# Optimization experiments

Hardware: AMD Instinct MI355X
Metric: run time of the kernel (lower is better)

The kernel has to match this reference:

```python
import jax, jax.numpy as jnp
import numpy as np

B, S, D_MODEL, N_HEADS, D_HEAD = 2, 2048, 2048, 16, 128


def _rope_tables(seq_len, d_head, base=10000.0):
    # standard llama RoPE cos/sin tables, broadcastable to (B, H, S, d_head)
    inv_freq = 1.0 / (base ** (np.arange(0, d_head, 2, dtype=np.float32) / d_head))
    t = np.arange(seq_len, dtype=np.float32)
    freqs = np.outer(t, inv_freq)                      # (S, d_head/2)
    emb = np.concatenate([freqs, freqs], axis=-1)       # (S, d_head)
    cos = jnp.asarray(np.cos(emb))[None, None]          # (1,1,S,d_head)
    sin = jnp.asarray(np.sin(emb))[None, None]
    return cos, sin


def setup_inputs() -> dict:
    key = jax.random.key(0)
    ks = jax.random.split(key, 5)
    scale = 0.02
    x = jax.random.normal(ks[0], (B, S, D_MODEL), dtype=jnp.float32)
    Wq = jax.random.normal(ks[1], (D_MODEL, D_MODEL), dtype=jnp.float32) * scale
    Wk = jax.random.normal(ks[2], (D_MODEL, D_MODEL), dtype=jnp.float32) * scale
    Wv = jax.random.normal(ks[3], (D_MODEL, D_MODEL), dtype=jnp.float32) * scale
    Wo = jax.random.normal(ks[4], (D_MODEL, D_MODEL), dtype=jnp.float32) * scale
    cos, sin = _rope_tables(S, D_HEAD)
    return {"x": x, "cos": cos, "sin": sin, "Wq": Wq, "Wk": Wk, "Wv": Wv, "Wo": Wo}


def _rotate_half(x):
    x1, x2 = jnp.split(x, 2, axis=-1)
    return jnp.concatenate([-x2, x1], axis=-1)


def _apply_rope(x, cos, sin):
    return x * cos + _rotate_half(x) * sin


def reference(x, cos, sin, Wq, Wk, Wv, Wo):
    b, s, _ = x.shape
    # QKV projections (nn.Linear computes x @ W.T), reshape to (B, H, S, Dh)
    def proj(W):
        return (x @ W.T).reshape(b, s, N_HEADS, D_HEAD).transpose(0, 2, 1, 3)
    q = _apply_rope(proj(Wq), cos, sin)
    k = _apply_rope(proj(Wk), cos, sin)
    v = proj(Wv)
    # causal scaled dot-product attention
    scale = 1.0 / jnp.sqrt(jnp.asarray(D_HEAD, dtype=x.dtype))
    scores = jnp.einsum("bhqd,bhkd->bhqk", q, k) * scale
    causal = jnp.tril(jnp.ones((s, s), dtype=bool))
    scores = jnp.where(causal, scores, jnp.asarray(-jnp.inf, dtype=scores.dtype))
    attn = jax.nn.softmax(scores, axis=-1)
    vals = jnp.einsum("bhqk,bhkd->bhqd", attn, v)
    vals = vals.transpose(0, 2, 1, 3).reshape(b, s, D_MODEL)
    return vals @ Wo.T
```

## Files before the change

### kernel.cpp

```cpp
#include <hip/hip_runtime.h>

#define S_LEN 2048
#define DMODEL 2048
#define NHEADS 16
#define DHEAD 128
#define BATCH 2

typedef unsigned short u16;
typedef __attribute__((ext_vector_type(8))) __bf16 bf16x8;
typedef __attribute__((ext_vector_type(4))) float f32x4;

__device__ __forceinline__ u16 f2bf(float f) {
    union { float f; unsigned int u; } a; a.f = f;
    unsigned int u = a.u;
    u += 0x7fffu + ((u >> 16) & 1u);
    return (u16)(u >> 16);
}
__device__ __forceinline__ u16 f2bf_fast(float f) {
    union { float f; unsigned int u; } a; a.f = f;
    return (u16)((a.u + 0x8000u) >> 16);
}
__device__ __forceinline__ float bf2f(u16 b) {
    union { unsigned int u; float f; } a; a.u = ((unsigned int)b) << 16;
    return a.f;
}

__device__ __forceinline__ void g2l16(const void* g, void* l) {
    __builtin_amdgcn_global_load_lds((const __attribute__((address_space(1))) unsigned int*)g,
                                     (__attribute__((address_space(3))) unsigned int*)l,
                                     16, 0, 0);
}

__global__ void cvt_bf16(const float* __restrict__ in, u16* __restrict__ out, int n4) {
    int i = blockIdx.x * 256 + threadIdx.x;
    if (i >= n4) return;
    f32x4 v = *(const f32x4*)(in + (size_t)i * 4);
    ushort4 o;
    o.x = f2bf(v[0]); o.y = f2bf(v[1]); o.z = f2bf(v[2]); o.w = f2bf(v[3]);
    *(ushort4*)(out + (size_t)i * 4) = o;
}

__global__ void cvt_w4(const float* __restrict__ w0, const float* __restrict__ w1,
                       const float* __restrict__ w2, const float* __restrict__ w3,
                       u16* __restrict__ dst, int n4) {
    int y = blockIdx.y;
    const float* src = (y == 0) ? w0 : (y == 1) ? w1 : (y == 2) ? w2 : w3;
    u16* out = dst + (size_t)y * DMODEL * DMODEL;
    int i = blockIdx.x * 256 + threadIdx.x;
    if (i >= n4) return;
    f32x4 v = *(const f32x4*)(src + (size_t)i * 4);
    ushort4 o;
    o.x = f2bf(v[0]); o.y = f2bf(v[1]); o.z = f2bf(v[2]); o.w = f2bf(v[3]);
    *(ushort4*)(out + (size_t)i * 4) = o;
}

#define QK_PRESCALE 0.12751744f
__global__ void rope_kernel(u16* __restrict__ Q, u16* __restrict__ K,
                            const float* __restrict__ cosT, const float* __restrict__ sinT) {
    u16* T = blockIdx.z ? K : Q;
    const float pre = blockIdx.z ? 1.0f : QK_PRESCALE;
    int bh = blockIdx.y;
    int t = blockIdx.x * 256 + threadIdx.x;
    int s = t >> 6;
    int d = t & 63;
    u16* row = T + ((size_t)bh * S_LEN + s) * DHEAD;
    float c  = cosT[s * DHEAD + d];
    float sn = sinT[s * DHEAD + d];
    float q1 = bf2f(row[d]);
    float q2 = bf2f(row[d + 64]);
    row[d]      = f2bf((q1 * c - q2 * sn) * pre);
    row[d + 64] = f2bf((q2 * c + q1 * sn) * pre);
}

__global__ __launch_bounds__(256) void gemm_qkv(const u16* __restrict__ A,
                                                const u16* __restrict__ W,
                                                u16* __restrict__ Qo,
                                                u16* __restrict__ Ko,
                                                u16* __restrict__ Vto) {
    __shared__ u16 As[128 * 32];
    __shared__ u16 Ws[128 * 32];
    const int tid  = threadIdx.x;
    const int lane = tid & 63;
    const int wave = tid >> 6;
    const int wm = wave >> 1, wn = wave & 1;
    const int col = lane & 15, quad = lane >> 4;
    const int blk = blockIdx.x;
    const int xcd = blk & 7;
    const int loc = blk >> 3;
    const int nb  = xcd * 6 + loc % 6;
    const int mb  = loc / 6;
    const int m0 = mb * 128, n0 = nb * 128;
    const int K = DMODEL;

    f32x4 acc[4][4] = {};

    const int swl = (quad ^ ((col >> 1) & 3)) * 8;
    int a_off[4], w_off[4];
    #pragma unroll
    for (int mi = 0; mi < 4; ++mi) a_off[mi] = (wm * 64 + mi * 16 + col) * 32 + swl;
    #pragma unroll
    for (int ni = 0; ni < 4; ++ni) w_off[ni] = (wn * 64 + ni * 16 + col) * 32 + swl;

    for (int kk = 0; kk < K; kk += 32) {
        #pragma unroll
        for (int i = 0; i < 2; ++i) {
            int c = i * 256 + tid;
            int row = c >> 2;
            int ko = (((c & 3) ^ ((c >> 3) & 3))) * 8;
            int cb = i * 256 + wave * 64;
            g2l16(A + (size_t)(m0 + row) * K + kk + ko, (void*)(As + cb * 8));
            g2l16(W + (size_t)(n0 + row) * K + kk + ko, (void*)(Ws + cb * 8));
        }
        __syncthreads();
        bf16x8 af[4], wf[4];
        #pragma unroll
        for (int mi = 0; mi < 4; ++mi) af[mi] = *(const bf16x8*)&As[a_off[mi]];
        #pragma unroll
        for (int ni = 0; ni < 4; ++ni) wf[ni] = *(const bf16x8*)&Ws[w_off[ni]];
        #pragma unroll
        for (int mi = 0; mi < 4; ++mi)
            #pragma unroll
            for (int ni = 0; ni < 4; ++ni)
                acc[mi][ni] = __builtin_amdgcn_mfma_f32_16x16x32_bf16(af[mi], wf[ni], acc[mi][ni], 0, 0, 0);
        __syncthreads();
    }

    const int which = n0 >> 11;
    if (which == 2) {
        #pragma unroll
        for (int mi = 0; mi < 4; ++mi) {
            #pragma unroll
            for (int ni = 0; ni < 4; ++ni) {
                int s0   = m0 + wm * 64 + mi * 16 + quad * 4;
                int ncol = (n0 & 2047) + wn * 64 + ni * 16 + col;
                int b = s0 >> 11, s = s0 & 2047;
                int h = ncol >> 7, d = ncol & 127;
                ushort4 o;
                o.x = f2bf(acc[mi][ni][0]); o.y = f2bf(acc[mi][ni][1]);
                o.z = f2bf(acc[mi][ni][2]); o.w = f2bf(acc[mi][ni][3]);
                *(ushort4*)&Vto[(((size_t)(b * NHEADS + h)) * DHEAD + d) * S_LEN + s] = o;
            }
        }
    } else {
        u16* out = which ? Ko : Qo;
        #pragma unroll
        for (int mi = 0; mi < 4; ++mi)
            #pragma unroll
            for (int ni = 0; ni < 4; ++ni)
                #pragma unroll
                for (int r = 0; r < 4; ++r) {
                    int row  = m0 + wm * 64 + mi * 16 + quad * 4 + r;
                    int ncol = (n0 & 2047) + wn * 64 + ni * 16 + col;
                    int b = row >> 11, s = row & 2047;
                    int h = ncol >> 7, d = ncol & 127;
                    out[(((size_t)(b * NHEADS + h)) * S_LEN + s) * DHEAD + d] = f2bf(acc[mi][ni][r]);
                }
    }
}

__global__ __launch_bounds__(256) void gemm_out(const u16* __restrict__ A,
                                                const u16* __restrict__ W,
                                                float* __restrict__ out) {
    __shared__ u16 As[128 * 32];
    __shared__ u16 Ws[128 * 32];
    const int tid  = threadIdx.x;
    const int lane = tid & 63;
    const int wave = tid >> 6;
    const int wm = wave >> 1, wn = wave & 1;
    const int col = lane & 15, quad = lane >> 4;
    const int blk = blockIdx.x;
    const int xcd = blk & 7;
    const int loc = blk >> 3;
    const int nb  = xcd * 2 + (loc & 1);
    const int mb  = loc >> 1;
    const int m0 = mb * 128, n0 = nb * 128;
    const int K = DMODEL;

    f32x4 acc[4][4] = {};

    const int swl = (quad ^ ((col >> 1) & 3)) * 8;
    int a_off[4], w_off[4];
    #pragma unroll
    for (int mi = 0; mi < 4; ++mi) a_off[mi] = (wm * 64 + mi * 16 + col) * 32 + swl;
    #pragma unroll
    for (int ni = 0; ni < 4; ++ni) w_off[ni] = (wn * 64 + ni * 16 + col) * 32 + swl;

    for (int kk = 0; kk < K; kk += 32) {
        #pragma unroll
        for (int i = 0; i < 2; ++i) {
            int c = i * 256 + tid;
            int row = c >> 2;
            int ko = (((c & 3) ^ ((c >> 3) & 3))) * 8;
            int cb = i * 256 + wave * 64;
            g2l16(A + (size_t)(m0 + row) * K + kk + ko, (void*)(As + cb * 8));
            g2l16(W + (size_t)(n0 + row) * K + kk + ko, (void*)(Ws + cb * 8));
        }
        __syncthreads();
        bf16x8 af[4], wf[4];
        #pragma unroll
        for (int mi = 0; mi < 4; ++mi) af[mi] = *(const bf16x8*)&As[a_off[mi]];
        #pragma unroll
        for (int ni = 0; ni < 4; ++ni) wf[ni] = *(const bf16x8*)&Ws[w_off[ni]];
        #pragma unroll
        for (int mi = 0; mi < 4; ++mi)
            #pragma unroll
            for (int ni = 0; ni < 4; ++ni)
                acc[mi][ni] = __builtin_amdgcn_mfma_f32_16x16x32_bf16(af[mi], wf[ni], acc[mi][ni], 0, 0, 0);
        __syncthreads();
    }

    #pragma unroll
    for (int mi = 0; mi < 4; ++mi)
        #pragma unroll
        for (int ni = 0; ni < 4; ++ni)
            #pragma unroll
            for (int r = 0; r < 4; ++r) {
                int row  = m0 + wm * 64 + mi * 16 + quad * 4 + r;
                int ncol = n0 + wn * 64 + ni * 16 + col;
                out[(size_t)row * DMODEL + ncol] = acc[mi][ni][r];
            }
}

__global__ __launch_bounds__(256) void attn_kernel(const u16* __restrict__ Q,
                                                   const u16* __restrict__ K,
                                                   const u16* __restrict__ Vt,
                                                   u16* __restrict__ Ao) {
    __shared__ u16 Ks[32 * 128];
    __shared__ u16 Vs[128 * 32];
    __shared__ u16 Ps[4][16 * 32];

    const int tid  = threadIdx.x;
    const int lane = tid & 63;
    const int wave = tid >> 6;
    const int col = lane & 15, quad = lane >> 4;
    const int xcd = blockIdx.x & 7;
    const int sub = (blockIdx.x >> 3) & 3;
    const int bh  = xcd * 4 + sub;
    const int qtile = 31 - (int)(blockIdx.x >> 5);
    const int b = bh >> 4, h = bh & 15;
    const int qb = qtile * 64;
    const int qw = qb + wave * 16;

    const u16* Qb = Q  + (size_t)bh * S_LEN * DHEAD;
    const u16* Kb = K  + (size_t)bh * S_LEN * DHEAD;
    const u16* Vb = Vt + (size_t)bh * DHEAD * S_LEN;

    bf16x8 qf[4];
    #pragma unroll
    for (int dc = 0; dc < 4; ++dc)
        qf[dc] = *(const bf16x8*)&Qb[(size_t)(qw + col) * DHEAD + dc * 32 + quad * 8];

    const int swl = (quad ^ ((col >> 1) & 3)) * 8;
    int koff[2][4];
    #pragma unroll
    for (int t = 0; t < 2; ++t)
        #pragma unroll
        for (int dc = 0; dc < 4; ++dc)
            koff[t][dc] = (t * 16 + col) * 128 + (((dc * 4 + quad) ^ (col & 7)) * 8);

    f32x4 accO[8] = {};
    float mrow = -1e30f, lrow = 0.0f;

    const int kend = qb + 64;
    for (int kb = 0; kb < kend; kb += 32) {
        #pragma unroll
        for (int i = 0; i < 2; ++i) {
            int c = tid + i * 256;
            int kr = c >> 4, ko = c & 15;
            *(f32x4*)&Ks[kr * 128 + ((ko ^ (kr & 7)) * 8)] =
                *(const f32x4*)&Kb[(size_t)(kb + kr) * DHEAD + ko * 8];
            int vr = c >> 2, vc = c & 3;
            *(f32x4*)&Vs[vr * 32 + (((vc ^ ((c >> 3) & 3))) * 8)] =
                *(const f32x4*)&Vb[(size_t)vr * S_LEN + kb + vc * 8];
        }
        __syncthreads();

        if (kb <= qw + 15) {
            f32x4 sc[2] = {};
            #pragma unroll
            for (int t = 0; t < 2; ++t)
                #pragma unroll
                for (int dc = 0; dc < 4; ++dc) {
                    bf16x8 kf = *(const bf16x8*)&Ks[koff[t][dc]];
                    sc[t] = __builtin_amdgcn_mfma_f32_16x16x32_bf16(kf, qf[dc], sc[t], 0, 0, 0);
                }

            const int q_g = qw + col;
            float sv[2][4];
            #pragma unroll
            for (int t = 0; t < 2; ++t)
                #pragma unroll
                for (int r = 0; r < 4; ++r) {
                    int k_g = kb + t * 16 + quad * 4 + r;
                    sv[t][r] = (k_g <= q_g) ? sc[t][r] : -1e30f;
                }

            float m01 = fmaxf(fmaxf(sv[0][0], sv[0][1]), fmaxf(sv[0][2], sv[0][3]));
            float m23 = fmaxf(fmaxf(sv[1][0], sv[1][1]), fmaxf(sv[1][2], sv[1][3]));
            float mloc = fmaxf(m01, m23);
            mloc = fmaxf(mloc, __shfl_xor(mloc, 16));
            mloc = fmaxf(mloc, __shfl_xor(mloc, 32));
            float mn = fmaxf(mrow, mloc);
            float al = exp2f(mrow - mn);

            float p[2][4], rloc = 0.0f;
            #pragma unroll
            for (int t = 0; t < 2; ++t)
                #pragma unroll
                for (int r = 0; r < 4; ++r) {
                    p[t][r] = exp2f(sv[t][r] - mn);
                    rloc += p[t][r];
                }
            rloc += __shfl_xor(rloc, 16);
            rloc += __shfl_xor(rloc, 32);
            lrow = lrow * al + rloc;
            mrow = mn;

            if (__any(al != 1.0f)) {
                float alb[4];
                #pragma unroll
                for (int r = 0; r < 4; ++r)
                    alb[r] = __shfl(al, quad * 4 + r);
                #pragma unroll
                for (int ni = 0; ni < 8; ++ni)
                    #pragma unroll
                    for (int r = 0; r < 4; ++r)
                        accO[ni][r] *= alb[r];
            }

            u16* P = Ps[wave];
            #pragma unroll
            for (int t = 0; t < 2; ++t) {
                ushort4 o;
                o.x = f2bf_fast(p[t][0]); o.y = f2bf_fast(p[t][1]);
                o.z = f2bf_fast(p[t][2]); o.w = f2bf_fast(p[t][3]);
                int chunk = t * 2 + (quad >> 1);
                *(ushort4*)&P[col * 32 + ((chunk ^ ((col >> 1) & 3)) * 8) + (quad & 1) * 4] = o;
            }
            asm volatile("s_waitcnt lgkmcnt(0)" ::: "memory");
            bf16x8 pf = *(const bf16x8*)&P[col * 32 + swl];

            #pragma unroll
            for (int ni = 0; ni < 8; ++ni) {
                bf16x8 vf = *(const bf16x8*)&Vs[(ni * 16 + col) * 32 + swl];
                accO[ni] = __builtin_amdgcn_mfma_f32_16x16x32_bf16(pf, vf, accO[ni], 0, 0, 0);
            }
        }
        __syncthreads();
    }

    float lb[4];
    #pragma unroll
    for (int r = 0; r < 4; ++r)
        lb[r] = 1.0f / __shfl(lrow, quad * 4 + r);
    #pragma unroll
    for (int ni = 0; ni < 8; ++ni)
        #pragma unroll
        for (int r = 0; r < 4; ++r) {
            int q_g = qw + quad * 4 + r;
            int d = ni * 16 + col;
            Ao[((size_t)(b * S_LEN + q_g)) * DMODEL + h * DHEAD + d] = f2bf(accO[ni][r] * lb[r]);
        }
}

extern "C" void kernel_launch(void* const* d_in, const int* in_sizes, int n_in,
                              void* d_out, int out_size, void* d_ws, size_t ws_size,
                              hipStream_t stream) {
    const float* x    = (const float*)d_in[0];
    const float* cosT = (const float*)d_in[1];
    const float* sinT = (const float*)d_in[2];
    const float* Wq   = (const float*)d_in[3];
    const float* Wk   = (const float*)d_in[4];
    const float* Wv   = (const float*)d_in[5];
    const float* Wo   = (const float*)d_in[6];

    char* ws = (char*)d_ws;
    size_t off = 0;
    auto carve = [&](size_t bytes) {
        void* p = ws + off;
        off += (bytes + 255) & ~(size_t)255;
        return p;
    };
    const size_t xN = (size_t)BATCH * S_LEN * DMODEL;
    const size_t wN = (size_t)DMODEL * DMODEL;
    u16* xb   = (u16*)carve(xN * 2);
    u16* wqkv = (u16*)carve(wN * 2 * 4);
    u16* wob  = wqkv + wN * 3;
    u16* Qb   = (u16*)carve(xN * 2);
    u16* Kb   = (u16*)carve(xN * 2);
    u16* Vtb  = (u16*)carve(xN * 2);
    u16* attn = xb;

    cvt_bf16<<<(int)(xN / 4 / 256), 256, 0, stream>>>(x, xb, (int)(xN / 4));
    cvt_w4<<<dim3((int)(wN / 4 / 256), 4), 256, 0, stream>>>(Wq, Wk, Wv, Wo, wqkv, (int)(wN / 4));

    gemm_qkv<<<dim3(1536), 256, 0, stream>>>(xb, wqkv, Qb, Kb, Vtb);

    rope_kernel<<<dim3(S_LEN * 64 / 256, BATCH * NHEADS, 2), 256, 0, stream>>>(Qb, Kb, cosT, sinT);

    attn_kernel<<<dim3(1024), 256, 0, stream>>>(Qb, Kb, Vtb, attn);

    gemm_out<<<dim3(512), 256, 0, stream>>>(attn, wob, (float*)d_out);
}
```

Baseline: 460.7 us.

## Fuse conversions, vectorize RoPE and QK stores, pad attention LDS instead of swizzle

Merges the x and weight fp32-to-bf16 conversions into one launch and vectorizes the RoPE kernel to four elements per thread. In gemm_qkv, the Q/K tiles swap operand roles so each lane holds consecutive head-dim values and can write packed ushort4 stores instead of scalar ones. The attention kernel replaces XOR-swizzled shared memory with padded row strides, which simplifies addressing but may change LDS bank-conflict behaviour.

```diff
diff --git a/kernel.cpp b/kernel.cpp
--- a/kernel.cpp
+++ b/kernel.cpp
@@ -31,21 +31,20 @@
                                      16, 0, 0);
 }
 
-__global__ void cvt_bf16(const float* __restrict__ in, u16* __restrict__ out, int n4) {
-    int i = blockIdx.x * 256 + threadIdx.x;
-    if (i >= n4) return;
-    f32x4 v = *(const f32x4*)(in + (size_t)i * 4);
-    ushort4 o;
-    o.x = f2bf(v[0]); o.y = f2bf(v[1]); o.z = f2bf(v[2]); o.w = f2bf(v[3]);
-    *(ushort4*)(out + (size_t)i * 4) = o;
-}
-
-__global__ void cvt_w4(const float* __restrict__ w0, const float* __restrict__ w1,
-                       const float* __restrict__ w2, const float* __restrict__ w3,
-                       u16* __restrict__ dst, int n4) {
+__global__ void cvt_all(const float* __restrict__ x,
+                        const float* __restrict__ w0, const float* __restrict__ w1,
+                        const float* __restrict__ w2, const float* __restrict__ w3,
+                        u16* __restrict__ xb, u16* __restrict__ wdst) {
     int y = blockIdx.y;
-    const float* src = (y == 0) ? w0 : (y == 1) ? w1 : (y == 2) ? w2 : w3;
-    u16* out = dst + (size_t)y * DMODEL * DMODEL;
+    const float* src;
+    u16* out;
+    int n4;
+    if (y == 0) { src = x; out = xb; n4 = (BATCH * S_LEN * DMODEL) / 4; }
+    else {
+        src = (y == 1) ? w0 : (y == 2) ? w1 : (y == 3) ? w2 : w3;
+        out = wdst + (size_t)(y - 1) * DMODEL * DMODEL;
+        n4 = (DMODEL * DMODEL) / 4;
+    }
     int i = blockIdx.x * 256 + threadIdx.x;
     if (i >= n4) return;
     f32x4 v = *(const f32x4*)(src + (size_t)i * 4);
@@ -61,15 +60,26 @@
     const float pre = blockIdx.z ? 1.0f : QK_PRESCALE;
     int bh = blockIdx.y;
     int t = blockIdx.x * 256 + threadIdx.x;
-    int s = t >> 6;
-    int d = t & 63;
+    int s = t >> 4;
+    int d4 = (t & 15) * 4;
     u16* row = T + ((size_t)bh * S_LEN + s) * DHEAD;
-    float c  = cosT[s * DHEAD + d];
-    float sn = sinT[s * DHEAD + d];
-    float q1 = bf2f(row[d]);
-    float q2 = bf2f(row[d + 64]);
-    row[d]      = f2bf((q1 * c - q2 * sn) * pre);
-    row[d + 64] = f2bf((q2 * c + q1 * sn) * pre);
+    ushort4 lo = *(ushort4*)&row[d4];
+    ushort4 hi = *(ushort4*)&row[d4 + 64];
+    f32x4 cv = *(const f32x4*)&cosT[s * DHEAD + d4];
+    f32x4 sv = *(const f32x4*)&sinT[s * DHEAD + d4];
+    float l0 = bf2f(lo.x), l1 = bf2f(lo.y), l2 = bf2f(lo.z), l3 = bf2f(lo.w);
+    float h0 = bf2f(hi.x), h1 = bf2f(hi.y), h2 = bf2f(hi.z), h3 = bf2f(hi.w);
+    ushort4 olo, ohi;
+    olo.x = f2bf((l0 * cv[0] - h0 * sv[0]) * pre);
+    olo.y = f2bf((l1 * cv[1] - h1 * sv[1]) * pre);
+    olo.z = f2bf((l2 * cv[2] - h2 * sv[2]) * pre);
+    olo.w = f2bf((l3 * cv[3] - h3 * sv[3]) * pre);
+    ohi.x = f2bf((h0 * cv[0] + l0 * sv[0]) * pre);
+    ohi.y = f2bf((h1 * cv[1] + l1 * sv[1]) * pre);
+    ohi.z = f2bf((h2 * cv[2] + l2 * sv[2]) * pre);
+    ohi.w = f2bf((h3 * cv[3] + l3 * sv[3]) * pre);
+    *(ushort4*)&row[d4]      = olo;
+    *(ushort4*)&row[d4 + 64] = ohi;
 }
 
 __global__ __launch_bounds__(256) void gemm_qkv(const u16* __restrict__ A,
@@ -91,6 +101,12 @@
     const int mb  = loc / 6;
     const int m0 = mb * 128, n0 = nb * 128;
     const int K = DMODEL;
+    const int which = n0 >> 11;
+
+    const u16* P0 = (which == 2) ? A : W;
+    const u16* P1 = (which == 2) ? W : A;
+    const int  r0 = (which == 2) ? m0 : n0;
+    const int  r1 = (which == 2) ? n0 : m0;
 
     f32x4 acc[4][4] = {};
 
@@ -108,8 +124,8 @@
             int row = c >> 2;
             int ko = (((c & 3) ^ ((c >> 3) & 3))) * 8;
             int cb = i * 256 + wave * 64;
-            g2l16(A + (size_t)(m0 + row) * K + kk + ko, (void*)(As + cb * 8));
-            g2l16(W + (size_t)(n0 + row) * K + kk + ko, (void*)(Ws + cb * 8));
+            g2l16(P0 + (size_t)(r0 + row) * K + kk + ko, (void*)(As + cb * 8));
+            g2l16(P1 + (size_t)(r1 + row) * K + kk + ko, (void*)(Ws + cb * 8));
         }
         __syncthreads();
         bf16x8 af[4], wf[4];
@@ -125,7 +141,6 @@
         __syncthreads();
     }
 
-    const int which = n0 >> 11;
     if (which == 2) {
         #pragma unroll
         for (int mi = 0; mi < 4; ++mi) {
@@ -144,17 +159,19 @@
     } else {
         u16* out = which ? Ko : Qo;
         #pragma unroll
-        for (int mi = 0; mi < 4; ++mi)
-            #pragma unroll
-            for (int ni = 0; ni < 4; ++ni)
-                #pragma unroll
-                for (int r = 0; r < 4; ++r) {
-                    int row  = m0 + wm * 64 + mi * 16 + quad * 4 + r;
-                    int ncol = (n0 & 2047) + wn * 64 + ni * 16 + col;
-                    int b = row >> 11, s = row & 2047;
-                    int h = ncol >> 7, d = ncol & 127;
-                    out[(((size_t)(b * NHEADS + h)) * S_LEN + s) * DHEAD + d] = f2bf(acc[mi][ni][r]);
-                }
+        for (int mi = 0; mi < 4; ++mi) {
+            #pragma unroll
+            for (int ni = 0; ni < 4; ++ni) {
+                int dd = (n0 & 2047) + wm * 64 + mi * 16 + quad * 4;
+                int sg = m0 + wn * 64 + ni * 16 + col;
+                int b = sg >> 11, s = sg & 2047;
+                int h = dd >> 7, d = dd & 127;
+                ushort4 o;
+                o.x = f2bf(acc[mi][ni][0]); o.y = f2bf(acc[mi][ni][1]);
+                o.z = f2bf(acc[mi][ni][2]); o.w = f2bf(acc[mi][ni][3]);
+                *(ushort4*)&out[(((size_t)(b * NHEADS + h)) * S_LEN + s) * DHEAD + d] = o;
+            }
+        }
     }
 }
 
@@ -225,9 +242,9 @@
                                                    const u16* __restrict__ K,
                                                    const u16* __restrict__ Vt,
                                                    u16* __restrict__ Ao) {
-    __shared__ u16 Ks[32 * 128];
-    __shared__ u16 Vs[128 * 32];
-    __shared__ u16 Ps[4][16 * 32];
+    __shared__ u16 Ks[32 * 136];
+    __shared__ u16 Vs[128 * 40];
+    __shared__ u16 Ps[4][16 * 40];
 
     const int tid  = threadIdx.x;
     const int lane = tid & 63;
@@ -250,14 +267,6 @@
     for (int dc = 0; dc < 4; ++dc)
         qf[dc] = *(const bf16x8*)&Qb[(size_t)(qw + col) * DHEAD + dc * 32 + quad * 8];
 
-    const int swl = (quad ^ ((col >> 1) & 3)) * 8;
-    int koff[2][4];
-    #pragma unroll
-    for (int t = 0; t < 2; ++t)
-        #pragma unroll
-        for (int dc = 0; dc < 4; ++dc)
-            koff[t][dc] = (t * 16 + col) * 128 + (((dc * 4 + quad) ^ (col & 7)) * 8);
-
     f32x4 accO[8] = {};
     float mrow = -1e30f, lrow = 0.0f;
 
@@ -266,12 +275,10 @@
         #pragma unroll
         for (int i = 0; i < 2; ++i) {
             int c = tid + i * 256;
-            int kr = c >> 4, ko = c & 15;
-            *(f32x4*)&Ks[kr * 128 + ((ko ^ (kr & 7)) * 8)] =
-                *(const f32x4*)&Kb[(size_t)(kb + kr) * DHEAD + ko * 8];
-            int vr = c >> 2, vc = c & 3;
-            *(f32x4*)&Vs[vr * 32 + (((vc ^ ((c >> 3) & 3))) * 8)] =
-                *(const f32x4*)&Vb[(size_t)vr * S_LEN + kb + vc * 8];
+            int kr = c >> 4, ko = (c & 15) * 8;
+            *(f32x4*)&Ks[kr * 136 + ko] = *(const f32x4*)&Kb[(size_t)(kb + kr) * DHEAD + ko];
+            int vr = c >> 2, vo = (c & 3) * 8;
+            *(f32x4*)&Vs[vr * 40 + vo] = *(const f32x4*)&Vb[(size_t)vr * S_LEN + kb + vo];
         }
         __syncthreads();
 
@@ -281,7 +288,7 @@
             for (int t = 0; t < 2; ++t)
                 #pragma unroll
                 for (int dc = 0; dc < 4; ++dc) {
-                    bf16x8 kf = *(const bf16x8*)&Ks[koff[t][dc]];
+                    bf16x8 kf = *(const bf16x8*)&Ks[(t * 16 + col) * 136 + dc * 32 + quad * 8];
                     sc[t] = __builtin_amdgcn_mfma_f32_16x16x32_bf16(kf, qf[dc], sc[t], 0, 0, 0);
                 }
 
@@ -334,15 +341,14 @@
                 ushort4 o;
                 o.x = f2bf_fast(p[t][0]); o.y = f2bf_fast(p[t][1]);
                 o.z = f2bf_fast(p[t][2]); o.w = f2bf_fast(p[t][3]);
-                int chunk = t * 2 + (quad >> 1);
-                *(ushort4*)&P[col * 32 + ((chunk ^ ((col >> 1) & 3)) * 8) + (quad & 1) * 4] = o;
+                *(ushort4*)&P[col * 40 + t * 16 + quad * 4] = o;
             }
             asm volatile("s_waitcnt lgkmcnt(0)" ::: "memory");
-            bf16x8 pf = *(const bf16x8*)&P[col * 32 + swl];
+            bf16x8 pf = *(const bf16x8*)&P[col * 40 + quad * 8];
 
             #pragma unroll
             for (int ni = 0; ni < 8; ++ni) {
-                bf16x8 vf = *(const bf16x8*)&Vs[(ni * 16 + col) * 32 + swl];
+                bf16x8 vf = *(const bf16x8*)&Vs[(ni * 16 + col) * 40 + quad * 8];
                 accO[ni] = __builtin_amdgcn_mfma_f32_16x16x32_bf16(pf, vf, accO[ni], 0, 0, 0);
             }
         }
@@ -391,12 +397,11 @@
     u16* Vtb  = (u16*)carve(xN * 2);
     u16* attn = xb;
 
-    cvt_bf16<<<(int)(xN / 4 / 256), 256, 0, stream>>>(x, xb, (int)(xN / 4));
-    cvt_w4<<<dim3((int)(wN / 4 / 256), 4), 256, 0, stream>>>(Wq, Wk, Wv, Wo, wqkv, (int)(wN / 4));
+    cvt_all<<<dim3(8192, 5), 256, 0, stream>>>(x, Wq, Wk, Wv, Wo, xb, wqkv);
 
     gemm_qkv<<<dim3(1536), 256, 0, stream>>>(xb, wqkv, Qb, Kb, Vtb);
 
-    rope_kernel<<<dim3(S_LEN * 64 / 256, BATCH * NHEADS, 2), 256, 0, stream>>>(Qb, Kb, cosT, sinT);
+    rope_kernel<<<dim3(S_LEN * 16 / 256, BATCH * NHEADS, 2), 256, 0, stream>>>(Qb, Kb, cosT, sinT);
 
     attn_kernel<<<dim3(1024), 256, 0, stream>>>(Qb, Kb, Vtb, attn);
 
```

Measured after the change: 418.9 us. 1.1x faster.
